# Performance work log

Hardware: AMD Instinct MI355X
Metric: run time of the kernel (lower is better)

Reference implementation:

```python
import jax, jax.numpy as jnp
import numpy as np

EPS = 1e-5

def rotate_half(x):
    # interleaved pairs: (..., d*2) -> stack(-x2, x1) interleaved back
    x = x.reshape(*x.shape[:-1], -1, 2)
    x1, x2 = x[..., 0], x[..., 1]
    return jnp.stack((-x2, x1), axis=-1).reshape(*x.shape[:-2], -1)

def apply_rotary(freqs, x):
    # freqs: (b, n, d); x: (b, h, n, d) -> broadcast over heads (unsqueeze at dim=1)
    f = freqs[:, None, :, :]
    return x * jnp.cos(f) + rotate_half(x) * jnp.sin(f)

def layer_norm(x, g, b):
    mu = jnp.mean(x, axis=-1, keepdims=True)
    var = jnp.var(x, axis=-1, keepdims=True)
    return (x - mu) * jax.lax.rsqrt(var + EPS) * g + b

def setup_inputs() -> dict:
    key = jax.random.key(0)
    ks = jax.random.split(key, 10)
    b, nq, nkv, dim, h, dh = 8, 1024, 2048, 512, 8, 64
    inner = h * dh
    return {
        "x_query": jax.random.normal(ks[0], (b, nq, dim), jnp.float32),
        "x_context": jax.random.normal(ks[1], (b, nkv, dim), jnp.float32),
        "rotary_time_emb_query": jax.random.normal(ks[2], (b, nq, dh), jnp.float32),
        "rotary_time_emb_context": jax.random.normal(ks[3], (b, nkv, dh), jnp.float32),
        "context_mask": jnp.ones((b, nkv), dtype=bool),
        "ln_q_g": jnp.ones((dim,), jnp.float32),
        "ln_q_b": jnp.zeros((dim,), jnp.float32),
        "ln_c_g": jnp.ones((dim,), jnp.float32),
        "ln_c_b": jnp.zeros((dim,), jnp.float32),
        "Wq": jax.random.normal(ks[4], (dim, inner), jnp.float32) * 0.02,
        "Wkv": jax.random.normal(ks[5], (dim, 2 * inner), jnp.float32) * 0.02,
        "Wo": jax.random.normal(ks[6], (inner, dim), jnp.float32) * 0.02,
        "bo": jnp.zeros((dim,), jnp.float32),
    }

def reference(x_query, x_context, rotary_time_emb_query, rotary_time_emb_context,
              context_mask, ln_q_g, ln_q_b, ln_c_g, ln_c_b, Wq, Wkv, Wo, bo):
    h = 8
    xq = layer_norm(x_query, ln_q_g, ln_q_b)
    xc = layer_norm(x_context, ln_c_g, ln_c_b)
    q = xq @ Wq                       # (b, nq, inner)
    kv = xc @ Wkv                     # (b, nkv, 2*inner)
    k, v = jnp.split(kv, 2, axis=-1)
    split_heads = lambda t: t.reshape(t.shape[0], t.shape[1], h, -1).transpose(0, 2, 1, 3)
    q, k, v = split_heads(q), split_heads(k), split_heads(v)  # (b, h, n, dh)
    q = apply_rotary(rotary_time_emb_query, q)
    k = apply_rotary(rotary_time_emb_context, k)
    v = apply_rotary(rotary_time_emb_context, v)   # rotate_value=True
    dh = q.shape[-1]
    scale = 1.0 / jnp.sqrt(jnp.float32(dh))
    scores = jnp.einsum('bhqd,bhkd->bhqk', q, k) * scale
    neg = jnp.finfo(scores.dtype).min
    scores = jnp.where(context_mask[:, None, None, :], scores, neg)
    attn = jax.nn.softmax(scores, axis=-1)
    out = jnp.einsum('bhqk,bhkd->bhqd', attn, v)
    out = apply_rotary(-rotary_time_emb_query, out)  # inverse rotation
    out = out.transpose(0, 2, 1, 3).reshape(out.shape[0], out.shape[2], -1)  # (b, nq, inner)
    return out @ Wo + bo
```

## Files before the change

kernel.cpp:

```cpp
#include <hip/hip_runtime.h>
#include <hip/hip_bf16.h>
#include <math.h>

#define BB 8
#define NQ 1024
#define NKV 2048
#define DIM 512
#define H 8
#define DH 64
#define INNER 512
#define SCALE_LOG2E 0.18033688011112042f

typedef __bf16 bf16x8 __attribute__((ext_vector_type(8)));
typedef float f32x4 __attribute__((ext_vector_type(4)));
typedef unsigned int u32x4 __attribute__((ext_vector_type(4)));

__device__ __forceinline__ unsigned short f2bf(float f) {
  union { float f; unsigned int u; } v; v.f = f;
  unsigned int r = v.u + 0x7fffu + ((v.u >> 16) & 1u);
  return (unsigned short)(r >> 16);
}
__device__ __forceinline__ float bf2f(unsigned short h) {
  union { unsigned int u; float f; } v; v.u = ((unsigned int)h) << 16;
  return v.f;
}

__device__ __forceinline__ void gl_lds16(const unsigned short* g, unsigned short* l) {
  __builtin_amdgcn_global_load_lds(
      (const __attribute__((address_space(1))) unsigned int*)g,
      (__attribute__((address_space(3))) unsigned int*)l, 16, 0, 0);
}

__global__ __launch_bounds__(256) void prep_ln(
    const float* __restrict__ Wq, const float* __restrict__ Wkv,
    const float* __restrict__ Wo,
    unsigned short* __restrict__ WqT, unsigned short* __restrict__ WkvT,
    unsigned short* __restrict__ WohT, unsigned short* __restrict__ WolT,
    const float* __restrict__ xq, const float* __restrict__ xc,
    const float* __restrict__ gq, const float* __restrict__ bq,
    const float* __restrict__ gc, const float* __restrict__ bc,
    unsigned short* __restrict__ xq_bf, unsigned short* __restrict__ xc_bf) {
  __shared__ float T[64][65];
  __shared__ float red[8];
  int blk = blockIdx.x;
  int t = threadIdx.x;
  if (blk < 2048) {
    int wid = t >> 6, lane = t & 63;
    for (int rr = 0; rr < 12; ++rr) {
      int row = blk * 12 + rr;
      const float* x; const float* g; const float* bbv; unsigned short* outp;
      if (row < BB * NQ) {
        x = xq + (size_t)row * DIM; g = gq; bbv = bq; outp = xq_bf + (size_t)row * DIM;
      } else {
        int r2 = row - BB * NQ;
        x = xc + (size_t)r2 * DIM; g = gc; bbv = bc; outp = xc_bf + (size_t)r2 * DIM;
      }
      float2 v = *reinterpret_cast<const float2*>(x + t * 2);
      float s = v.x + v.y;
      float ss = v.x * v.x + v.y * v.y;
#pragma unroll
      for (int d = 1; d < 64; d <<= 1) { s += __shfl_xor(s, d); ss += __shfl_xor(ss, d); }
      if (lane == 0) { red[wid] = s; red[4 + wid] = ss; }
      __syncthreads();
      s = red[0] + red[1] + red[2] + red[3];
      ss = red[4] + red[5] + red[6] + red[7];
      __syncthreads();
      float mu = s * (1.0f / DIM);
      float var = ss * (1.0f / DIM) - mu * mu;
      float rs = rsqrtf(var + 1e-5f);
      float y0 = (v.x - mu) * rs * g[t * 2] + bbv[t * 2];
      float y1 = (v.y - mu) * rs * g[t * 2 + 1] + bbv[t * 2 + 1];
      ushort2 o; o.x = f2bf(y0); o.y = f2bf(y1);
      *reinterpret_cast<ushort2*>(outp + t * 2) = o;
    }
  } else {
    int blk2 = blk - 2048;
    const float* src; int Wd, ti, tj, mode;
    unsigned short* dst = nullptr;
    if (blk2 < 64) { src = Wq;  dst = WqT;  Wd = 512;  ti = blk2 >> 3; tj = blk2 & 7; mode = 0; }
    else if (blk2 < 192) { int b2 = blk2 - 64; src = Wkv; dst = WkvT; Wd = 1024; ti = b2 >> 4; tj = b2 & 15; mode = 0; }
    else { int b2 = blk2 - 192; src = Wo; Wd = 512; ti = b2 >> 3; tj = b2 & 7; mode = 1; }
#pragma unroll
    for (int i = 0; i < 16; ++i) {
      int idx = i * 256 + t;
      int r = idx >> 6, c = idx & 63;
      T[r][c] = src[(size_t)(ti * 64 + r) * Wd + tj * 64 + c];
    }
    __syncthreads();
#pragma unroll
    for (int i = 0; i < 16; ++i) {
      int idx = i * 256 + t;
      int n = idx >> 6, k = idx & 63;
      float v = T[k][n];
      size_t off = (size_t)(tj * 64 + n) * 512 + ti * 64 + k;
      if (mode == 0) {
        dst[off] = f2bf(v);
      } else {
        unsigned short hb = f2bf(v);
        WohT[off] = hb;
        WolT[off] = f2bf(v - bf2f(hb));
      }
    }
  }
}

__device__ __forceinline__ void gemm128_mainloop(
    const unsigned short* __restrict__ A, const unsigned short* __restrict__ WT,
    unsigned short* As, unsigned short* Ws,
    int rowBase, int colBase, f32x4 acc[4][4]) {
  const int t = threadIdx.x;
  const int w = t >> 6, l = t & 63;
  const int l15 = l & 15, lg = l >> 4, c7 = l15 & 7;
  const int wr = w >> 1, wc = w & 1;
  const int lrow = l >> 3;
  const int lchunk = (l & 7) ^ lrow;
  const int frag = (lg ^ c7) * 8;
  const unsigned short* Ag = A + (size_t)rowBase * 512;
  const unsigned short* Wg = WT + (size_t)colBase * 512;
#pragma unroll
  for (int m = 0; m < 4; ++m)
#pragma unroll
    for (int n = 0; n < 4; ++n) acc[m][n] = f32x4{0.f, 0.f, 0.f, 0.f};
  for (int kb = 0; kb < 512; kb += 64) {
#pragma unroll
    for (int i = 0; i < 4; ++i) {
      const int seg = w * 4 + i;
      const size_t goff = (size_t)(seg * 8 + lrow) * 512 + kb + lchunk * 8;
      gl_lds16(Ag + goff, As + seg * 512);
      gl_lds16(Wg + goff, Ws + seg * 512);
    }
    __syncthreads();
#pragma unroll
    for (int ks = 0; ks < 2; ++ks) {
      const int xo = ks ? 32 : 0;
      bf16x8 af[4], bf_[4];
#pragma unroll
      for (int m = 0; m < 4; ++m)
        af[m] = *reinterpret_cast<const bf16x8*>(
            &As[(wr * 64 + m * 16 + l15) * 64 + (frag ^ xo)]);
#pragma unroll
      for (int n = 0; n < 4; ++n)
        bf_[n] = *reinterpret_cast<const bf16x8*>(
            &Ws[(wc * 64 + n * 16 + l15) * 64 + (frag ^ xo)]);
#pragma unroll
      for (int m = 0; m < 4; ++m)
#pragma unroll
        for (int n = 0; n < 4; ++n)
          acc[m][n] = __builtin_amdgcn_mfma_f32_16x16x32_bf16(af[m], bf_[n], acc[m][n], 0, 0, 0);
    }
    __syncthreads();
  }
}

__global__ __launch_bounds__(256) void proj_fused(
    const unsigned short* __restrict__ xq_bf, const unsigned short* __restrict__ xc_bf,
    const unsigned short* __restrict__ WqT, const unsigned short* __restrict__ WkvT,
    const float* __restrict__ rotq, const float* __restrict__ rotc,
    const int* __restrict__ cmask,
    unsigned short* __restrict__ Qb, unsigned short* __restrict__ Kb,
    unsigned short* __restrict__ VTb) {
  __shared__ __align__(16) char smem[128 * 66 * 4];
  unsigned short* As = (unsigned short*)smem;
  unsigned short* Ws = (unsigned short*)(smem + 16384);
  float (*Cs)[66] = (float(*)[66])smem;
  const int t = threadIdx.x;
  const int w = t >> 6, l = t & 63;
  const int l15 = l & 15, lg = l >> 4;
  const int wr = w >> 1, wc = w & 1;
  f32x4 acc[4][4];
  int o = blockIdx.x;
  if (o < 1024) {
    int swz = ((o & 7) << 7) | (o >> 3);
    int bn = swz & 7, bm = swz >> 3;
    gemm128_mainloop(xc_bf, WkvT, As, Ws, bm * 128, bn * 128, acc);
#pragma unroll
    for (int hc = 0; hc < 2; ++hc) {
      if (wc == hc) {
#pragma unroll
        for (int m = 0; m < 4; ++m)
#pragma unroll
          for (int n = 0; n < 4; ++n)
#pragma unroll
            for (int r = 0; r < 4; ++r)
              Cs[wr * 64 + m * 16 + lg * 4 + r][n * 16 + l15] = acc[m][n][r];
      }
      __syncthreads();
      const int g = bn * 2 + hc;
      const int h = g & 7;
      if (g < 8) {
#pragma unroll
        for (int i = 0; i < 16; ++i) {
          int p = i * 256 + t;
          int row = p >> 5, pc = p & 31, d0 = pc * 2;
          int grow = bm * 128 + row;
          float c0 = Cs[row][d0], c1 = Cs[row][d0 + 1];
          const float* f = rotc + (size_t)grow * DH + d0;
          float f0 = f[0], f1 = f[1], s0, s1, co0, co1;
          __sincosf(f0, &s0, &co0);
          __sincosf(f1, &s1, &co1);
          float mf = cmask[grow] ? 1.f : 0.f;
          float o0 = (c0 * co0 - c1 * s0) * mf;
          float o1 = (c1 * co1 + c0 * s1) * mf;
          int b = grow >> 11, kk = grow & 2047;
          ushort2 ov; ov.x = f2bf(o0); ov.y = f2bf(o1);
          *reinterpret_cast<ushort2*>(Kb + (((size_t)(b * H + h) * NKV + kk) * DH + d0)) = ov;
        }
      } else {
        int oc = t & 7;
        int dd0 = t >> 3;
#pragma unroll
        for (int ch = 0; ch < 2; ++ch) {
          int ch64 = bm * 2 + ch;
          int bb = ch64 >> 5, chunk = ch64 & 31;
          unsigned short* vbase = VTb + (((size_t)(bb * H + h) * 32 + chunk) * 64) * 64;
#pragma unroll
          for (int half = 0; half < 2; ++half) {
            int d = dd0 + half * 32;
            u32x4 pack;
#pragma unroll
            for (int j2 = 0; j2 < 4; ++j2) {
              unsigned int lohi[2];
#pragma unroll
              for (int e = 0; e < 2; ++e) {
                int p = oc * 8 + j2 * 2 + e;
                int pp = p & 31;
                int kv = (p >> 5) * 32 + ((pp & 1) ? ((pp >> 1) + 16) : (pp >> 1));
                float c0 = Cs[ch * 64 + kv][d], cx = Cs[ch * 64 + kv][d ^ 1];
                float f = rotc[(size_t)(ch64 * 64 + kv) * DH + d];
                float sn, cs;
                __sincosf(f, &sn, &cs);
                float mf = cmask[ch64 * 64 + kv] ? 1.f : 0.f;
                float val = ((d & 1) ? (c0 * cs + cx * sn) : (c0 * cs - cx * sn)) * mf;
                lohi[e] = f2bf(val);
              }
              pack[j2] = lohi[0] | (lohi[1] << 16);
            }
            *reinterpret_cast<u32x4*>(vbase + d * 64 + oc * 8) = pack;
          }
        }
      }
      __syncthreads();
    }
  } else {
    int o2 = o - 1024;
    int swz = ((o2 & 7) << 5) | (o2 >> 3);
    int bn = swz & 3, bm = swz >> 2;
    gemm128_mainloop(xq_bf, WqT, As, Ws, bm * 128, bn * 128, acc);
#pragma unroll
    for (int hc = 0; hc < 2; ++hc) {
      if (wc == hc) {
#pragma unroll
        for (int m = 0; m < 4; ++m)
#pragma unroll
          for (int n = 0; n < 4; ++n)
#pragma unroll
            for (int r = 0; r < 4; ++r)
              Cs[wr * 64 + m * 16 + lg * 4 + r][n * 16 + l15] = acc[m][n][r];
      }
      __syncthreads();
      const int head = bn * 2 + hc;
#pragma unroll
      for (int i = 0; i < 16; ++i) {
        int p = i * 256 + t;
        int row = p >> 5, pc = p & 31, d0 = pc * 2;
        int grow = bm * 128 + row;
        float c0 = Cs[row][d0], c1 = Cs[row][d0 + 1];
        const float* f = rotq + (size_t)grow * DH + d0;
        float f0 = f[0], f1 = f[1], s0, s1, co0, co1;
        __sincosf(f0, &s0, &co0);
        __sincosf(f1, &s1, &co1);
        float o0 = (c0 * co0 - c1 * s0) * SCALE_LOG2E;
        float o1 = (c1 * co1 + c0 * s1) * SCALE_LOG2E;
        ushort2 ov; ov.x = f2bf(o0); ov.y = f2bf(o1);
        int b = grow >> 10, qq = grow & 1023;
        *reinterpret_cast<ushort2*>(Qb + (((size_t)(b * H + head) * NQ + qq) * DH + d0)) = ov;
      }
      __syncthreads();
    }
  }
}

__global__ __launch_bounds__(256) void attn_kernel(
    const unsigned short* __restrict__ Qb, const unsigned short* __restrict__ Kb,
    const unsigned short* __restrict__ VTb, const int* __restrict__ mask,
    const float* __restrict__ rotq,
    unsigned short* __restrict__ Ahb, unsigned short* __restrict__ Alb) {
  __shared__ unsigned short Ks[2 * 64 * 64];
  __shared__ unsigned short Vs[2 * 64 * 64];
  __shared__ unsigned short Ps[4 * 16 * 64];
  int ob = blockIdx.x;
  int swz = ((ob & 7) << 7) + (ob >> 3);
  int qb = swz & 15;
  int bh = swz >> 4;
  int b = bh >> 3, hh = bh & 7;
  int t = threadIdx.x, w = t >> 6, l = t & 63;
  int l15 = l & 15, lg = l >> 4;
  int c7 = l15 & 7;

  float nmasked;
  {
    const int* mrow = mask + b * NKV;
    float msum = 0.f;
#pragma unroll
    for (int i = 0; i < 8; ++i) {
      int4 m = *reinterpret_cast<const int4*>(mrow + l * 4 + i * 256);
      msum += (m.x ? 1.f : 0.f) + (m.y ? 1.f : 0.f) +
              (m.z ? 1.f : 0.f) + (m.w ? 1.f : 0.f);
    }
#pragma unroll
    for (int d = 1; d < 64; d <<= 1) msum += __shfl_xor(msum, d);
    nmasked = (float)NKV - msum;
  }

  const unsigned short* qrow = Qb + ((size_t)bh * NQ + qb * 64 + w * 16 + l15) * DH;
  bf16x8 qa0 = *reinterpret_cast<const bf16x8*>(qrow + lg * 8);
  bf16x8 qa1 = *reinterpret_cast<const bf16x8*>(qrow + 32 + lg * 8);

  float plsum[4] = {0.f, 0.f, 0.f, 0.f};
  f32x4 acc[4];
#pragma unroll
  for (int ct = 0; ct < 4; ++ct) acc[ct] = f32x4{0.f, 0.f, 0.f, 0.f};

  const int srow = t >> 2;
  const int sseg = (t & 3) * 16;
  const int sdst0 = srow * 64 + ((2 * (t & 3)) ^ (srow & 7)) * 8;
  const int frag = (lg ^ c7) * 8;
  const int kbase = l15 * 64 + frag;
  const int prbase = w * 1024 + l15 * 64 + frag;
  unsigned int* pw = reinterpret_cast<unsigned int*>(Ps);
  const int lg4 = lg * 4, l3 = l15 & 3, sD = l15 >> 2;

  const unsigned short* gk = Kb + ((size_t)bh * NKV + srow) * DH + sseg;
  const unsigned short* gv = VTb + (((size_t)bh * 32) * 64 + srow) * 64 + sseg;

  bf16x8 kr0 = *reinterpret_cast<const bf16x8*>(gk);
  bf16x8 kr1 = *reinterpret_cast<const bf16x8*>(gk + 8);
  bf16x8 vr0 = *reinterpret_cast<const bf16x8*>(gv);
  bf16x8 vr1 = *reinterpret_cast<const bf16x8*>(gv + 8);
  gk += 4096; gv += 4096;

#pragma unroll 2
  for (int ic = 0; ic < NKV / 64; ++ic) {
    const int bo_ = (ic & 1) << 12;
    *reinterpret_cast<bf16x8*>(&Ks[bo_ + sdst0])       = kr0;
    *reinterpret_cast<bf16x8*>(&Ks[bo_ + (sdst0 ^ 8)]) = kr1;
    *reinterpret_cast<bf16x8*>(&Vs[bo_ + sdst0])       = vr0;
    *reinterpret_cast<bf16x8*>(&Vs[bo_ + (sdst0 ^ 8)]) = vr1;
    __syncthreads();
    if (ic + 1 < NKV / 64) {
      kr0 = *reinterpret_cast<const bf16x8*>(gk);
      kr1 = *reinterpret_cast<const bf16x8*>(gk + 8);
      vr0 = *reinterpret_cast<const bf16x8*>(gv);
      vr1 = *reinterpret_cast<const bf16x8*>(gv + 8);
      gk += 4096; gv += 4096;
    }
    f32x4 s[4];
    __builtin_amdgcn_s_setprio(1);
#pragma unroll
    for (int tt = 0; tt < 4; ++tt) {
      f32x4 z = f32x4{0.f, 0.f, 0.f, 0.f};
      bf16x8 k0 = *reinterpret_cast<const bf16x8*>(&Ks[bo_ + tt * 1024 + kbase]);
      z = __builtin_amdgcn_mfma_f32_16x16x32_bf16(qa0, k0, z, 0, 0, 0);
      bf16x8 k1 = *reinterpret_cast<const bf16x8*>(&Ks[bo_ + tt * 1024 + (kbase ^ 32)]);
      z = __builtin_amdgcn_mfma_f32_16x16x32_bf16(qa1, k1, z, 0, 0, 0);
      s[tt] = z;
    }
    __builtin_amdgcn_s_setprio(0);
    float p[4][4];
#pragma unroll
    for (int tt = 0; tt < 4; ++tt)
#pragma unroll
      for (int r = 0; r < 4; ++r) {
        float e;
        asm("v_exp_f32 %0, %1" : "=v"(e) : "v"(s[tt][r]));
        p[tt][r] = e;
      }
#pragma unroll
    for (int r = 0; r < 4; ++r)
      plsum[r] += (p[0][r] + p[1][r]) + (p[2][r] + p[3][r]);
#pragma unroll
    for (int r = 0; r < 4; ++r) {
      unsigned int d01, d23;
      asm("v_cvt_pk_bf16_f32 %0, %1, %2" : "=v"(d01) : "v"(p[0][r]), "v"(p[1][r]));
      asm("v_cvt_pk_bf16_f32 %0, %1, %2" : "=v"(d23) : "v"(p[2][r]), "v"(p[3][r]));
      int row = lg4 + r;
      int rb = row & 7;
      int dwl = ((sD ^ rb) << 2) + l3;
      int pb = w * 512 + row * 32 + dwl;
      pw[pb] = d01;
      pw[pb ^ 16] = d23;
    }
    asm volatile("s_waitcnt lgkmcnt(0)" ::: "memory");
    __builtin_amdgcn_sched_barrier(0);
    __builtin_amdgcn_s_setprio(1);
#pragma unroll
    for (int ks = 0; ks < 2; ++ks) {
      bf16x8 pa = *reinterpret_cast<const bf16x8*>(&Ps[(prbase ^ (ks ? 32 : 0))]);
#pragma unroll
      for (int ct = 0; ct < 4; ++ct) {
        bf16x8 vb = *reinterpret_cast<const bf16x8*>(
            &Vs[bo_ + ct * 1024 + (kbase ^ (ks ? 32 : 0))]);
        acc[ct] = __builtin_amdgcn_mfma_f32_16x16x32_bf16(pa, vb, acc[ct], 0, 0, 0);
      }
    }
    __builtin_amdgcn_s_setprio(0);
  }
#pragma unroll
  for (int d = 1; d < 16; d <<= 1)
#pragma unroll
    for (int r = 0; r < 4; ++r) plsum[r] += __shfl_xor(plsum[r], d);
  float inv[4];
#pragma unroll
  for (int r = 0; r < 4; ++r) inv[r] = 1.0f / (plsum[r] - nmasked);

  int q0 = qb * 64 + w * 16 + lg * 4;
#pragma unroll
  for (int r = 0; r < 4; ++r) {
    int grow = b * NQ + q0 + r;
    const float* frow = rotq + (size_t)grow * DH;
    size_t obase = (size_t)grow * INNER + hh * DH;
#pragma unroll
    for (int ct = 0; ct < 4; ++ct) {
      int d = ct * 16 + l15;
      float x = acc[ct][r] * inv[r];
      float nb = __shfl_xor(x, 1);
      float f = frow[d];
      float sn, cs;
      __sincosf(f, &sn, &cs);
      float ov = (d & 1) ? (x * cs - nb * sn) : (x * cs + nb * sn);
      unsigned short hb = f2bf(ov);
      Ahb[obase + d] = hb;
      Alb[obase + d] = f2bf(ov - bf2f(hb));
    }
  }
}

__global__ __launch_bounds__(256) void final_gemm(
    const unsigned short* __restrict__ Ah, const unsigned short* __restrict__ Al,
    const unsigned short* __restrict__ Wh, const unsigned short* __restrict__ Wl,
    const float* __restrict__ bo, float* __restrict__ out) {
  __shared__ __align__(16) char smem[49152];
  unsigned short* AhS = (unsigned short*)smem;
  unsigned short* AlS = (unsigned short*)(smem + 16384);
  unsigned short* WhS = (unsigned short*)(smem + 32768);
  unsigned short* WlS = (unsigned short*)(smem + 40960);
  int o = blockIdx.x;
  int swz = ((o & 7) << 6) | (o >> 3);
  int bn = swz & 7, bm = swz >> 3;
  const int t = threadIdx.x;
  const int w = t >> 6, l = t & 63;
  const int l15 = l & 15, lg = l >> 4, c7 = l15 & 7;
  const int wr = w >> 1, wc = w & 1;
  const int lrow = l >> 3;
  const int lchunk = (l & 7) ^ lrow;
  const int frag = (lg ^ c7) * 8;
  const unsigned short* Agh = Ah + (size_t)bm * 128 * 512;
  const unsigned short* Agl = Al + (size_t)bm * 128 * 512;
  const unsigned short* Wgh = Wh + (size_t)bn * 64 * 512;
  const unsigned short* Wgl = Wl + (size_t)bn * 64 * 512;
  f32x4 acc[4][2];
#pragma unroll
  for (int m = 0; m < 4; ++m)
#pragma unroll
    for (int n = 0; n < 2; ++n) acc[m][n] = f32x4{0.f, 0.f, 0.f, 0.f};
  for (int kb = 0; kb < 512; kb += 64) {
#pragma unroll
    for (int i = 0; i < 4; ++i) {
      const int seg = w * 4 + i;
      const size_t goff = (size_t)(seg * 8 + lrow) * 512 + kb + lchunk * 8;
      gl_lds16(Agh + goff, AhS + seg * 512);
      gl_lds16(Agl + goff, AlS + seg * 512);
    }
#pragma unroll
    for (int i = 0; i < 2; ++i) {
      const int seg = w * 2 + i;
      const size_t goff = (size_t)(seg * 8 + lrow) * 512 + kb + lchunk * 8;
      gl_lds16(Wgh + goff, WhS + seg * 512);
      gl_lds16(Wgl + goff, WlS + seg * 512);
    }
    __syncthreads();
#pragma unroll
    for (int ks = 0; ks < 2; ++ks) {
      const int xo = ks ? 32 : 0;
      bf16x8 ah[4], al[4], wh[2], wl[2];
#pragma unroll
      for (int m = 0; m < 4; ++m) {
        const int off = (wr * 64 + m * 16 + l15) * 64 + (frag ^ xo);
        ah[m] = *reinterpret_cast<const bf16x8*>(&AhS[off]);
        al[m] = *reinterpret_cast<const bf16x8*>(&AlS[off]);
      }
#pragma unroll
      for (int n = 0; n < 2; ++n) {
        const int off = (wc * 32 + n * 16 + l15) * 64 + (frag ^ xo);
        wh[n] = *reinterpret_cast<const bf16x8*>(&WhS[off]);
        wl[n] = *reinterpret_cast<const bf16x8*>(&WlS[off]);
      }
#pragma unroll
      for (int m = 0; m < 4; ++m)
#pragma unroll
        for (int n = 0; n < 2; ++n) {
          acc[m][n] = __builtin_amdgcn_mfma_f32_16x16x32_bf16(ah[m], wh[n], acc[m][n], 0, 0, 0);
          acc[m][n] = __builtin_amdgcn_mfma_f32_16x16x32_bf16(al[m], wh[n], acc[m][n], 0, 0, 0);
          acc[m][n] = __builtin_amdgcn_mfma_f32_16x16x32_bf16(ah[m], wl[n], acc[m][n], 0, 0, 0);
        }
    }
    __syncthreads();
  }
  const int row0 = bm * 128 + wr * 64;
  const int col0 = bn * 64 + wc * 32;
#pragma unroll
  for (int m = 0; m < 4; ++m)
#pragma unroll
    for (int n = 0; n < 2; ++n) {
      int col = col0 + n * 16 + l15;
      float bv = bo[col];
#pragma unroll
      for (int r = 0; r < 4; ++r)
        out[(size_t)(row0 + m * 16 + lg * 4 + r) * 512 + col] = acc[m][n][r] + bv;
    }
}

extern "C" void kernel_launch(void* const* d_in, const int* in_sizes, int n_in,
                              void* d_out, int out_size, void* d_ws, size_t ws_size,
                              hipStream_t stream) {
  const float* x_query   = (const float*)d_in[0];
  const float* x_context = (const float*)d_in[1];
  const float* rot_q     = (const float*)d_in[2];
  const float* rot_c     = (const float*)d_in[3];
  const int*   cmask     = (const int*)d_in[4];
  const float* ln_q_g    = (const float*)d_in[5];
  const float* ln_q_b    = (const float*)d_in[6];
  const float* ln_c_g    = (const float*)d_in[7];
  const float* ln_c_b    = (const float*)d_in[8];
  const float* Wq        = (const float*)d_in[9];
  const float* Wkv       = (const float*)d_in[10];
  const float* Wo        = (const float*)d_in[11];
  const float* bo        = (const float*)d_in[12];
  float* out = (float*)d_out;

  char* ws = (char*)d_ws;
  unsigned short* xq_bf = (unsigned short*)(ws + 0);
  unsigned short* xc_bf = (unsigned short*)(ws + 8388608);
  unsigned short* Ahb   = (unsigned short*)(ws + 0);
  unsigned short* Alb   = (unsigned short*)(ws + 8388608);
  unsigned short* WqT   = (unsigned short*)(ws + 25165824);
  unsigned short* WkvT  = (unsigned short*)(ws + 25690112);
  unsigned short* Qb    = (unsigned short*)(ws + 26738688);
  unsigned short* Kb    = (unsigned short*)(ws + 35127296);
  unsigned short* VTb   = (unsigned short*)(ws + 51904512);
  unsigned short* WohT  = (unsigned short*)(ws + 68681728);
  unsigned short* WolT  = (unsigned short*)(ws + 69206016);

  prep_ln<<<dim3(2304), dim3(256), 0, stream>>>(
      Wq, Wkv, Wo, WqT, WkvT, WohT, WolT,
      x_query, x_context, ln_q_g, ln_q_b, ln_c_g, ln_c_b, xq_bf, xc_bf);
  proj_fused<<<dim3(1280), dim3(256), 0, stream>>>(
      xq_bf, xc_bf, WqT, WkvT, rot_q, rot_c, cmask, Qb, Kb, VTb);
  attn_kernel<<<dim3(1024), dim3(256), 0, stream>>>(Qb, Kb, VTb, cmask, rot_q, Ahb, Alb);
  final_gemm<<<dim3(512), dim3(256), 0, stream>>>(Ahb, Alb, WohT, WolT, bo, out);
}
```

Baseline: 146.4 us.

## Keep attention probabilities in registers by computing transposed QK^T scores

Swaps the MFMA operands for the score computation so each lane holds scores for a single query row across several keys. This lets the exponentiated probabilities be packed directly into the A operand of the PV MFMA. The shared-memory P staging buffer, its stores, the lgkmcnt wait and the sched barrier are removed, and the row-sum reduction changes to a different shuffle pattern. The intent is to cut LDS traffic and a sync point from the inner loop. It relies on the transposed register layout matching the MFMA A-operand layout for the k dimension.

After: 142.9 us. 2.4% less time.

```diff
diff --git a/kernel.cpp b/kernel.cpp
--- a/kernel.cpp
+++ b/kernel.cpp
@@ -287,7 +287,6 @@
     unsigned short* __restrict__ Ahb, unsigned short* __restrict__ Alb) {
   __shared__ unsigned short Ks[2 * 64 * 64];
   __shared__ unsigned short Vs[2 * 64 * 64];
-  __shared__ unsigned short Ps[4 * 16 * 64];
   int ob = blockIdx.x;
   int swz = ((ob & 7) << 7) + (ob >> 3);
   int qb = swz & 15;
@@ -316,7 +315,7 @@
   bf16x8 qa0 = *reinterpret_cast<const bf16x8*>(qrow + lg * 8);
   bf16x8 qa1 = *reinterpret_cast<const bf16x8*>(qrow + 32 + lg * 8);
 
-  float plsum[4] = {0.f, 0.f, 0.f, 0.f};
+  float plsum = 0.f;
   f32x4 acc[4];
 #pragma unroll
   for (int ct = 0; ct < 4; ++ct) acc[ct] = f32x4{0.f, 0.f, 0.f, 0.f};
@@ -326,9 +325,6 @@
   const int sdst0 = srow * 64 + ((2 * (t & 3)) ^ (srow & 7)) * 8;
   const int frag = (lg ^ c7) * 8;
   const int kbase = l15 * 64 + frag;
-  const int prbase = w * 1024 + l15 * 64 + frag;
-  unsigned int* pw = reinterpret_cast<unsigned int*>(Ps);
-  const int lg4 = lg * 4, l3 = l15 & 3, sD = l15 >> 2;
 
   const unsigned short* gk = Kb + ((size_t)bh * NKV + srow) * DH + sseg;
   const unsigned short* gv = VTb + (((size_t)bh * 32) * 64 + srow) * 64 + sseg;
@@ -360,9 +356,9 @@
     for (int tt = 0; tt < 4; ++tt) {
       f32x4 z = f32x4{0.f, 0.f, 0.f, 0.f};
       bf16x8 k0 = *reinterpret_cast<const bf16x8*>(&Ks[bo_ + tt * 1024 + kbase]);
-      z = __builtin_amdgcn_mfma_f32_16x16x32_bf16(qa0, k0, z, 0, 0, 0);
+      z = __builtin_amdgcn_mfma_f32_16x16x32_bf16(k0, qa0, z, 0, 0, 0);
       bf16x8 k1 = *reinterpret_cast<const bf16x8*>(&Ks[bo_ + tt * 1024 + (kbase ^ 32)]);
-      z = __builtin_amdgcn_mfma_f32_16x16x32_bf16(qa1, k1, z, 0, 0, 0);
+      z = __builtin_amdgcn_mfma_f32_16x16x32_bf16(k1, qa1, z, 0, 0, 0);
       s[tt] = z;
     }
     __builtin_amdgcn_s_setprio(0);
@@ -375,43 +371,33 @@
         asm("v_exp_f32 %0, %1" : "=v"(e) : "v"(s[tt][r]));
         p[tt][r] = e;
       }
-#pragma unroll
-    for (int r = 0; r < 4; ++r)
-      plsum[r] += (p[0][r] + p[1][r]) + (p[2][r] + p[3][r]);
-#pragma unroll
-    for (int r = 0; r < 4; ++r) {
-      unsigned int d01, d23;
-      asm("v_cvt_pk_bf16_f32 %0, %1, %2" : "=v"(d01) : "v"(p[0][r]), "v"(p[1][r]));
-      asm("v_cvt_pk_bf16_f32 %0, %1, %2" : "=v"(d23) : "v"(p[2][r]), "v"(p[3][r]));
-      int row = lg4 + r;
-      int rb = row & 7;
-      int dwl = ((sD ^ rb) << 2) + l3;
-      int pb = w * 512 + row * 32 + dwl;
-      pw[pb] = d01;
-      pw[pb ^ 16] = d23;
-    }
-    asm volatile("s_waitcnt lgkmcnt(0)" ::: "memory");
-    __builtin_amdgcn_sched_barrier(0);
+    plsum += ((p[0][0] + p[0][1]) + (p[0][2] + p[0][3])) +
+             ((p[1][0] + p[1][1]) + (p[1][2] + p[1][3])) +
+             ((p[2][0] + p[2][1]) + (p[2][2] + p[2][3])) +
+             ((p[3][0] + p[3][1]) + (p[3][2] + p[3][3]));
     __builtin_amdgcn_s_setprio(1);
 #pragma unroll
     for (int ks = 0; ks < 2; ++ks) {
-      bf16x8 pa = *reinterpret_cast<const bf16x8*>(&Ps[(prbase ^ (ks ? 32 : 0))]);
+      union { u32x4 u; bf16x8 b; } pa;
+#pragma unroll
+      for (int i = 0; i < 4; ++i)
+        asm("v_cvt_pk_bf16_f32 %0, %1, %2"
+            : "=v"(pa.u[i]) : "v"(p[ks * 2][i]), "v"(p[ks * 2 + 1][i]));
 #pragma unroll
       for (int ct = 0; ct < 4; ++ct) {
         bf16x8 vb = *reinterpret_cast<const bf16x8*>(
             &Vs[bo_ + ct * 1024 + (kbase ^ (ks ? 32 : 0))]);
-        acc[ct] = __builtin_amdgcn_mfma_f32_16x16x32_bf16(pa, vb, acc[ct], 0, 0, 0);
+        acc[ct] = __builtin_amdgcn_mfma_f32_16x16x32_bf16(pa.b, vb, acc[ct], 0, 0, 0);
       }
     }
     __builtin_amdgcn_s_setprio(0);
   }
-#pragma unroll
-  for (int d = 1; d < 16; d <<= 1)
-#pragma unroll
-    for (int r = 0; r < 4; ++r) plsum[r] += __shfl_xor(plsum[r], d);
+  plsum += __shfl_xor(plsum, 16);
+  plsum += __shfl_xor(plsum, 32);
   float inv[4];
 #pragma unroll
-  for (int r = 0; r < 4; ++r) inv[r] = 1.0f / (plsum[r] - nmasked);
+  for (int r = 0; r < 4; ++r)
+    inv[r] = 1.0f / (__shfl(plsum, lg * 4 + r) - nmasked);
 
   int q0 = qb * 64 + w * 16 + lg * 4;
 #pragma unroll
```
